# Kernel tuning notes

Measured on AMD Instinct MI355X. Metric: run time of the kernel, lower is better.

The kernel has to match this reference:

```python
import jax, jax.numpy as jnp
import numpy as np

B, S, H, NH = 4, 2048, 768, 12
HD = H // NH

def _ln(x, g, b, eps=1e-5):
    m = jnp.mean(x, -1, keepdims=True)
    v = jnp.mean((x - m) ** 2, -1, keepdims=True)
    return (x - m) * jax.lax.rsqrt(v + eps) * g + b

def setup_inputs() -> dict:
    key = jax.random.key(0)
    ks = jax.random.split(key, 16)
    s = 0.02
    return {
        "x": jax.random.normal(ks[0], (B, S, H), jnp.float32),
        "prev_state": jax.random.normal(ks[1], (B, S, H), jnp.float32),
        "mask": jax.random.randint(ks[2], (B,), 0, 2).astype(bool),
        # depthwise conv1d (groups=H, k=3): torch weight [H, 1, 3] == OIH
        "conv_dw_w": jax.random.normal(ks[3], (H, 1, 3), jnp.float32) * s,
        "conv_dw_b": jnp.zeros((H,), jnp.float32),
        # pointwise conv1d (k=1) stored as [out, in]
        "conv_pw_w": jax.random.normal(ks[4], (H, H), jnp.float32) * s,
        "conv_pw_b": jnp.zeros((H,), jnp.float32),
        "cn_g": jnp.ones((H,), jnp.float32), "cn_b": jnp.zeros((H,), jnp.float32),
        "Wq": jax.random.normal(ks[5], (H, H), jnp.float32) * s, "bq": jnp.zeros((H,), jnp.float32),
        "Wk": jax.random.normal(ks[6], (H, H), jnp.float32) * s, "bk": jnp.zeros((H,), jnp.float32),
        "Wv": jax.random.normal(ks[7], (H, H), jnp.float32) * s, "bv": jnp.zeros((H,), jnp.float32),
        "Wo": jax.random.normal(ks[8], (H, H), jnp.float32) * s, "bo": jnp.zeros((H,), jnp.float32),
        "pn_g": jnp.ones((H,), jnp.float32), "pn_b": jnp.zeros((H,), jnp.float32),
        "Wpost": jax.random.normal(ks[9], (H, H), jnp.float32) * s, "bpost": jnp.zeros((H,), jnp.float32),
        "Wg": jax.random.normal(ks[10], (1, 2 * H), jnp.float32) * s, "bg": jnp.zeros((1,), jnp.float32),
    }

def reference(x, prev_state, mask, conv_dw_w, conv_dw_b, conv_pw_w, conv_pw_b,
              cn_g, cn_b, Wq, bq, Wk, bk, Wv, bv, Wo, bo,
              pn_g, pn_b, Wpost, bpost, Wg, bg):
    # ---- bridge: depthwise conv (k=3) -> pointwise conv (k=1) -> GELU -> LN ----
    mem_t = prev_state.transpose(0, 2, 1)  # [B, H, S]
    dw = jax.lax.conv_general_dilated(
        mem_t, conv_dw_w, window_strides=(1,), padding=[(1, 1)],
        feature_group_count=H, dimension_numbers=("NCH", "OIH", "NCH")) + conv_dw_b[None, :, None]
    pw = jnp.einsum("bhs,oh->bos", dw, conv_pw_w) + conv_pw_b[None, :, None]
    bridged = jax.nn.gelu(pw, approximate=False).transpose(0, 2, 1)  # [B, S, H]
    bridged = _ln(bridged, cn_g, cn_b)
    # ---- cross attention: q from x, k/v from bridged memory (nope, non-causal) ----
    q = (jnp.einsum("bsh,oh->bso", x, Wq) + bq).reshape(B, S, NH, HD)
    k = (jnp.einsum("bsh,oh->bso", bridged, Wk) + bk).reshape(B, S, NH, HD)
    v = (jnp.einsum("bsh,oh->bso", bridged, Wv) + bv).reshape(B, S, NH, HD)
    scores = jnp.einsum("bqnd,bknd->bnqk", q, k) / np.float32(np.sqrt(HD))
    attn = jax.nn.softmax(scores, axis=-1)
    ao = jnp.einsum("bnqk,bknd->bqnd", attn, v).reshape(B, S, H)
    ao = jnp.einsum("bsh,oh->bso", ao, Wo) + bo
    # ---- post-attn norm, linear, gate, scatter-add back under mask ----
    inj = _ln(ao, pn_g, pn_b)
    inj = jnp.einsum("bsh,oh->bso", inj, Wpost) + bpost
    gate = jax.nn.sigmoid(jnp.einsum("bsh,oh->bso", jnp.concatenate([x, bridged], -1), Wg) + bg)
    gated = gate * jnp.tanh(inj)
    mf = mask.astype(x.dtype)[:, None, None]  # batch-row select == masked scatter-add
    out = x + mf * gated
    # masked MSE aux loss (only over selected rows, as in the original)
    denom = jnp.maximum(mask.sum(), 1).astype(x.dtype) * np.float32(S * H)
    aux = jnp.sum(mf * (bridged - x) ** 2) / denom
    return out, aux
```

## Files before the change

### kernel.cpp

```cpp
#include <hip/hip_runtime.h>
#include <math.h>

#define B_ 4
#define S_ 2048
#define H_ 768
#define NH_ 12
#define HD_ 64
#define BSH (B_ * S_ * H_)
#define NROWS (B_ * S_)
#define WSZ (H_ * H_)

typedef __attribute__((ext_vector_type(8))) short bf16x8;
typedef __attribute__((ext_vector_type(4))) short s16x4;
typedef __attribute__((ext_vector_type(4))) float f32x4;
typedef __attribute__((ext_vector_type(2))) unsigned u32x2;

__device__ __forceinline__ short f2bf(float f) {
  union { float f; unsigned u; } x; x.f = f;
  unsigned r = x.u + 0x7FFF + ((x.u >> 16) & 1);
  return (short)(r >> 16);
}
__device__ __forceinline__ float bf2f(short s) {
  union { unsigned u; float f; } x;
  x.u = ((unsigned)(unsigned short)s) << 16;
  return x.f;
}
__device__ __forceinline__ unsigned bfpack(float lo, float hi) {
  union { float f; unsigned u; } a, b; a.f = lo; b.f = hi;
  return __builtin_amdgcn_perm(b.u, a.u, 0x07060302);
}

typedef __attribute__((address_space(1))) const unsigned int g_u32;
typedef __attribute__((address_space(3))) unsigned int l_u32;
__device__ __forceinline__ void gload16(const void* g, void* l) {
  __builtin_amdgcn_global_load_lds((g_u32*)g, (l_u32*)l, 16, 0, 0);
}

__global__ __launch_bounds__(256) void cvt_x_k(const float* __restrict__ src,
                                               short* __restrict__ dst) {
  int i = (blockIdx.x * 256 + threadIdx.x) * 4;
  float4 v = *(const float4*)(src + i);
  s16x4 o = {f2bf(v.x), f2bf(v.y), f2bf(v.z), f2bf(v.w)};
  *(s16x4*)(dst + i) = o;
}

__global__ __launch_bounds__(256) void cvt6_k(const float* w0, const float* w1,
                                              const float* w2, const float* w3,
                                              const float* w4, const float* w5,
                                              short* __restrict__ dst) {
  int i = (blockIdx.x * 256 + threadIdx.x) * 4;
  int m = i / WSZ;
  int off = i - m * WSZ;
  const float* s = m == 0 ? w0 : m == 1 ? w1 : m == 2 ? w2 : m == 3 ? w3 : m == 4 ? w4 : w5;
  float4 v = *(const float4*)(s + off);
  s16x4 o = {f2bf(v.x), f2bf(v.y), f2bf(v.z), f2bf(v.w)};
  *(s16x4*)(dst + i) = o;
}

__global__ __launch_bounds__(192) void dwconv_k(const float* __restrict__ prev,
                                                const float* __restrict__ w3,
                                                const float* __restrict__ bias,
                                                short* __restrict__ out) {
  int row = blockIdx.x;
  int s = row & (S_ - 1);
  int h = threadIdx.x * 4;
  size_t base = (size_t)row * H_ + h;
  float4 c = *(const float4*)(prev + base);
  float4 wa = *(const float4*)(w3 + h * 3);
  float4 wb = *(const float4*)(w3 + h * 3 + 4);
  float4 wc = *(const float4*)(w3 + h * 3 + 8);
  float4 bi = *(const float4*)(bias + h);
  float4 acc;
  acc.x = bi.x + c.x * wa.y;
  acc.y = bi.y + c.y * wb.x;
  acc.z = bi.z + c.z * wb.w;
  acc.w = bi.w + c.w * wc.z;
  if (s > 0) {
    float4 l = *(const float4*)(prev + base - H_);
    acc.x += l.x * wa.x; acc.y += l.y * wa.w; acc.z += l.z * wb.z; acc.w += l.w * wc.y;
  }
  if (s < S_ - 1) {
    float4 r = *(const float4*)(prev + base + H_);
    acc.x += r.x * wa.z; acc.y += r.y * wb.y; acc.z += r.z * wc.x; acc.w += r.w * wc.w;
  }
  s16x4 o = {f2bf(acc.x), f2bf(acc.y), f2bf(acc.z), f2bf(acc.w)};
  *(s16x4*)(out + base) = o;
}

struct GemmJob {
  const short* A; const short* W; const float* bias; short* C; int act; int tout;
};

__global__ __launch_bounds__(256) void gemm_bf2(GemmJob j0, GemmJob j1, GemmJob j2) {
  GemmJob j = blockIdx.z == 0 ? j0 : (blockIdx.z == 1 ? j1 : j2);
  __shared__ short As[128 * 64];
  __shared__ short Ws[128 * 64];
  int tid = threadIdx.x, lane = tid & 63, w = tid >> 6;
  int wr = w >> 1, wc = w & 1, lm = lane & 15, lq = lane >> 4;
  int m0 = blockIdx.y * 128, n0 = blockIdx.x * 128;
  int srow = lane >> 3;
  int skc = (lane & 7) * 8;
  const short* gA = j.A + (size_t)(m0 + w * 32 + srow) * H_ + skc;
  const short* gW = j.W + (size_t)(n0 + w * 32 + srow) * H_ + skc;
  short* lA = As + w * 2048;
  short* lW = Ws + w * 2048;

  f32x4 acc[4][4];
#pragma unroll
  for (int i = 0; i < 4; ++i)
#pragma unroll
    for (int jj = 0; jj < 4; ++jj) acc[i][jj] = (f32x4){0.f, 0.f, 0.f, 0.f};

  for (int kt = 0; kt < H_; kt += 64) {
    __syncthreads();
#pragma unroll
    for (int c = 0; c < 4; ++c) {
      gload16(gA + kt + (size_t)(c * 8) * H_, lA + c * 512);
      gload16(gW + kt + (size_t)(c * 8) * H_, lW + c * 512);
    }
    __syncthreads();
#pragma unroll
    for (int kk = 0; kk < 2; ++kk) {
      bf16x8 af[4], wf[4];
#pragma unroll
      for (int i = 0; i < 4; ++i)
        af[i] = *(const bf16x8*)&As[(wr * 64 + i * 16 + lm) * 64 + kk * 32 + lq * 8];
#pragma unroll
      for (int jj = 0; jj < 4; ++jj)
        wf[jj] = *(const bf16x8*)&Ws[(wc * 64 + jj * 16 + lm) * 64 + kk * 32 + lq * 8];
#pragma unroll
      for (int i = 0; i < 4; ++i)
#pragma unroll
        for (int jj = 0; jj < 4; ++jj)
          acc[i][jj] = __builtin_amdgcn_mfma_f32_16x16x32_bf16(af[i], wf[jj], acc[i][jj], 0, 0, 0);
    }
  }

  if (!j.tout) {
#pragma unroll
    for (int jj = 0; jj < 4; ++jj) {
      int col = n0 + wc * 64 + jj * 16 + lm;
      float bn = j.bias[col];
#pragma unroll
      for (int i = 0; i < 4; ++i) {
        int mrow = m0 + wr * 64 + i * 16 + lq * 4;
#pragma unroll
        for (int r = 0; r < 4; ++r) {
          float cv = acc[i][jj][r] + bn;
          if (j.act) cv = 0.5f * cv * (1.0f + erff(cv * 0.70710678118f));
          j.C[(size_t)(mrow + r) * H_ + col] = f2bf(cv);
        }
      }
    }
  } else {
    int b = m0 >> 11;
    int sb = (m0 & (S_ - 1)) + wr * 64;
#pragma unroll
    for (int jj = 0; jj < 4; ++jj) {
      int col = n0 + wc * 64 + jj * 16 + lm;
      float bn = j.bias[col];
      short* cp = j.C + ((size_t)(b * H_ + col)) * S_;
#pragma unroll
      for (int i = 0; i < 4; ++i) {
        int s = sb + i * 16 + lq * 4;
        s16x4 pk = {f2bf(acc[i][jj][0] + bn), f2bf(acc[i][jj][1] + bn),
                    f2bf(acc[i][jj][2] + bn), f2bf(acc[i][jj][3] + bn)};
        *(s16x4*)(cp + s) = pk;
      }
    }
  }
}

__global__ __launch_bounds__(256) void gemm_n64(const short* __restrict__ A,
                                                const short* __restrict__ W,
                                                const float* __restrict__ bias,
                                                short* __restrict__ C, int act) {
  __shared__ short As[128 * 64];
  __shared__ short Ws[64 * 64];
  int tid = threadIdx.x, lane = tid & 63, w = tid >> 6;
  int wm = w >> 1, wn = w & 1, lm = lane & 15, lq = lane >> 4;
  int m0 = blockIdx.y * 128, n0 = blockIdx.x * 64;
  const short* gA = A + (size_t)(m0 + w * 32 + (lane >> 3)) * H_ + (lane & 7) * 8;
  const short* gW = W + (size_t)(n0 + w * 16 + (lane >> 3)) * H_ + (lane & 7) * 8;
  short* lA = As + w * 2048;
  short* lW = Ws + w * 1024;

  f32x4 acc[4][2];
#pragma unroll
  for (int i = 0; i < 4; ++i)
#pragma unroll
    for (int jj = 0; jj < 2; ++jj) acc[i][jj] = (f32x4){0.f, 0.f, 0.f, 0.f};

  for (int kt = 0; kt < H_; kt += 64) {
    __syncthreads();
#pragma unroll
    for (int c = 0; c < 4; ++c)
      gload16(gA + kt + (size_t)(c * 8) * H_, lA + c * 512);
#pragma unroll
    for (int c = 0; c < 2; ++c)
      gload16(gW + kt + (size_t)(c * 8) * H_, lW + c * 512);
    __syncthreads();
#pragma unroll
    for (int kk = 0; kk < 2; ++kk) {
      bf16x8 af[4], wf[2];
#pragma unroll
      for (int i = 0; i < 4; ++i)
        af[i] = *(const bf16x8*)&As[(wm * 64 + i * 16 + lm) * 64 + kk * 32 + lq * 8];
#pragma unroll
      for (int jj = 0; jj < 2; ++jj)
        wf[jj] = *(const bf16x8*)&Ws[(wn * 32 + jj * 16 + lm) * 64 + kk * 32 + lq * 8];
#pragma unroll
      for (int i = 0; i < 4; ++i)
#pragma unroll
        for (int jj = 0; jj < 2; ++jj)
          acc[i][jj] = __builtin_amdgcn_mfma_f32_16x16x32_bf16(af[i], wf[jj], acc[i][jj], 0, 0, 0);
    }
  }

#pragma unroll
  for (int jj = 0; jj < 2; ++jj) {
    int col = n0 + wn * 32 + jj * 16 + lm;
    float bn = bias[col];
#pragma unroll
    for (int i = 0; i < 4; ++i) {
      int mrow = m0 + wm * 64 + i * 16 + lq * 4;
#pragma unroll
      for (int r = 0; r < 4; ++r) {
        float cv = acc[i][jj][r] + bn;
        if (act) cv = 0.5f * cv * (1.0f + erff(cv * 0.70710678118f));
        C[(size_t)(mrow + r) * H_ + col] = f2bf(cv);
      }
    }
  }
}

__global__ __launch_bounds__(256) void ln_bf(const short* __restrict__ X,
                                             short* __restrict__ Y,
                                             const float* __restrict__ g,
                                             const float* __restrict__ bb) {
  int row = blockIdx.x;
  size_t base = (size_t)row * H_;
  int h0 = threadIdx.x, h1 = h0 + 256, h2 = h0 + 512;
  float x0 = bf2f(X[base + h0]), x1 = bf2f(X[base + h1]), x2 = bf2f(X[base + h2]);
  float s = x0 + x1 + x2;
  float s2 = x0 * x0 + x1 * x1 + x2 * x2;
  for (int off = 32; off > 0; off >>= 1) {
    s += __shfl_down(s, off);
    s2 += __shfl_down(s2, off);
  }
  __shared__ float sa[4], sq[4], st[2];
  int wid = threadIdx.x >> 6, lane = threadIdx.x & 63;
  if (lane == 0) { sa[wid] = s; sq[wid] = s2; }
  __syncthreads();
  if (threadIdx.x == 0) {
    float ts = sa[0] + sa[1] + sa[2] + sa[3];
    float ts2 = sq[0] + sq[1] + sq[2] + sq[3];
    float mean = ts * (1.0f / H_);
    float var = ts2 * (1.0f / H_) - mean * mean;
    st[0] = mean;
    st[1] = rsqrtf(var + 1e-5f);
  }
  __syncthreads();
  float mean = st[0], rstd = st[1];
  Y[base + h0] = f2bf((x0 - mean) * rstd * g[h0] + bb[h0]);
  Y[base + h1] = f2bf((x1 - mean) * rstd * g[h1] + bb[h1]);
  Y[base + h2] = f2bf((x2 - mean) * rstd * g[h2] + bb[h2]);
}

__global__ __launch_bounds__(256) void attn4_k(const short* __restrict__ qb,
                                               const short* __restrict__ kb,
                                               const short* __restrict__ vtb,
                                               short* __restrict__ aob) {
  __shared__ short Ks[64 * 72];
  __shared__ short Vt[64 * 72];
  __shared__ short Ps[128 * 72];
  int tid = threadIdx.x, lane = tid & 63, w = tid >> 6;
  int lm = lane & 15, lq = lane >> 4;
  int b = blockIdx.z, n = blockIdx.y, q0 = blockIdx.x * 128;
  int hoff = n * HD_;

  bf16x8 qf[2][2];
#pragma unroll
  for (int qg = 0; qg < 2; ++qg) {
    const short* qrow = qb + ((size_t)(b * S_ + q0 + w * 32 + qg * 16 + lm)) * H_ + hoff;
    qf[qg][0] = *(const bf16x8*)(qrow + lq * 8);
    qf[qg][1] = *(const bf16x8*)(qrow + 32 + lq * 8);
  }

  float l_[2] = {0.f, 0.f};
  f32x4 o[4][2];
#pragma unroll
  for (int i = 0; i < 4; ++i)
#pragma unroll
    for (int qg = 0; qg < 2; ++qg) o[i][qg] = (f32x4){0.f, 0.f, 0.f, 0.f};

  int r0 = tid >> 2, c0 = (tid & 3) * 16;
  const short* kg = kb + ((size_t)(b * S_)) * H_ + hoff;
  const short* vg = vtb + ((size_t)(b * H_ + hoff)) * S_;
  const float C1 = 0.1803368802f;

  bf16x8 kv0 = *(const bf16x8*)(kg + (size_t)r0 * H_ + c0);
  bf16x8 kv1 = *(const bf16x8*)(kg + (size_t)r0 * H_ + c0 + 8);
  bf16x8 vv0 = *(const bf16x8*)(vg + (size_t)r0 * S_ + c0);
  bf16x8 vv1 = *(const bf16x8*)(vg + (size_t)r0 * S_ + c0 + 8);

  for (int kt = 0; kt < S_; kt += 64) {
    __syncthreads();
    *(bf16x8*)&Ks[r0 * 72 + c0] = kv0;
    *(bf16x8*)&Ks[r0 * 72 + c0 + 8] = kv1;
    *(bf16x8*)&Vt[r0 * 72 + c0] = vv0;
    *(bf16x8*)&Vt[r0 * 72 + c0 + 8] = vv1;
    __syncthreads();
    if (kt + 64 < S_) {
      kv0 = *(const bf16x8*)(kg + (size_t)(kt + 64 + r0) * H_ + c0);
      kv1 = *(const bf16x8*)(kg + (size_t)(kt + 64 + r0) * H_ + c0 + 8);
      vv0 = *(const bf16x8*)(vg + (size_t)r0 * S_ + kt + 64 + c0);
      vv1 = *(const bf16x8*)(vg + (size_t)r0 * S_ + kt + 64 + c0 + 8);
    }

    f32x4 st[4][2];
#pragma unroll
    for (int ni = 0; ni < 4; ++ni) {
      bf16x8 ka0 = *(const bf16x8*)&Ks[(ni * 16 + lm) * 72 + lq * 8];
      bf16x8 ka1 = *(const bf16x8*)&Ks[(ni * 16 + lm) * 72 + 32 + lq * 8];
#pragma unroll
      for (int qg = 0; qg < 2; ++qg) {
        f32x4 z = (f32x4){0.f, 0.f, 0.f, 0.f};
        z = __builtin_amdgcn_mfma_f32_16x16x32_bf16(ka0, qf[qg][0], z, 0, 0, 0);
        st[ni][qg] = __builtin_amdgcn_mfma_f32_16x16x32_bf16(ka1, qf[qg][1], z, 0, 0, 0);
      }
    }

#pragma unroll
    for (int qg = 0; qg < 2; ++qg) {
      float rs = 0.f;
#pragma unroll
      for (int ni = 0; ni < 4; ++ni) {
        float p0 = exp2f(st[ni][qg][0] * C1);
        float p1 = exp2f(st[ni][qg][1] * C1);
        float p2 = exp2f(st[ni][qg][2] * C1);
        float p3 = exp2f(st[ni][qg][3] * C1);
        rs += (p0 + p1) + (p2 + p3);
        u32x2 pk = {bfpack(p0, p1), bfpack(p2, p3)};
        *(u32x2*)&Ps[(w * 32 + qg * 16 + lm) * 72 + ni * 16 + lq * 4] = pk;
      }
      rs += __shfl_xor(rs, 16);
      rs += __shfl_xor(rs, 32);
      l_[qg] += rs;
    }

    bf16x8 pf[2][2];
#pragma unroll
    for (int qg = 0; qg < 2; ++qg) {
      pf[qg][0] = *(const bf16x8*)&Ps[(w * 32 + qg * 16 + lm) * 72 + lq * 8];
      pf[qg][1] = *(const bf16x8*)&Ps[(w * 32 + qg * 16 + lm) * 72 + 32 + lq * 8];
    }
#pragma unroll
    for (int nd = 0; nd < 4; ++nd) {
      bf16x8 va0 = *(const bf16x8*)&Vt[(nd * 16 + lm) * 72 + lq * 8];
      bf16x8 va1 = *(const bf16x8*)&Vt[(nd * 16 + lm) * 72 + 32 + lq * 8];
#pragma unroll
      for (int qg = 0; qg < 2; ++qg) {
        o[nd][qg] = __builtin_amdgcn_mfma_f32_16x16x32_bf16(va0, pf[qg][0], o[nd][qg], 0, 0, 0);
        o[nd][qg] = __builtin_amdgcn_mfma_f32_16x16x32_bf16(va1, pf[qg][1], o[nd][qg], 0, 0, 0);
      }
    }
  }

#pragma unroll
  for (int qg = 0; qg < 2; ++qg) {
    float inv = 1.0f / l_[qg];
    short* orow = aob + ((size_t)(b * S_ + q0 + w * 32 + qg * 16 + lm)) * H_ + hoff;
#pragma unroll
    for (int nd = 0; nd < 4; ++nd) {
      s16x4 pk = {f2bf(o[nd][qg][0] * inv), f2bf(o[nd][qg][1] * inv),
                  f2bf(o[nd][qg][2] * inv), f2bf(o[nd][qg][3] * inv)};
      *(s16x4*)(orow + nd * 16 + lq * 4) = pk;
    }
  }
}

__global__ __launch_bounds__(192) void gate_out_k(const float* __restrict__ x,
                                                  const short* __restrict__ br,
                                                  const short* __restrict__ inj,
                                                  const int* __restrict__ mask,
                                                  const float* __restrict__ Wg,
                                                  const float* __restrict__ bg,
                                                  float* __restrict__ out,
                                                  float* __restrict__ paux) {
  int row = blockIdx.x;
  int b = row >> 11;
  size_t base = (size_t)row * H_;
  int h = threadIdx.x * 4;
  float4 xv = *(const float4*)(x + base + h);
  s16x4 brv = *(const s16x4*)(br + base + h);
  s16x4 inv = *(const s16x4*)(inj + base + h);
  float4 wg0 = *(const float4*)(Wg + h);
  float4 wg1 = *(const float4*)(Wg + H_ + h);
  float b0 = bf2f(brv.x), b1 = bf2f(brv.y), b2 = bf2f(brv.z), b3 = bf2f(brv.w);
  float dot = xv.x * wg0.x + xv.y * wg0.y + xv.z * wg0.z + xv.w * wg0.w
            + b0 * wg1.x + b1 * wg1.y + b2 * wg1.z + b3 * wg1.w;
  float d0 = b0 - xv.x, d1 = b1 - xv.y, d2 = b2 - xv.z, d3 = b3 - xv.w;
  float aux = d0 * d0 + d1 * d1 + d2 * d2 + d3 * d3;
  for (int off = 32; off > 0; off >>= 1) {
    dot += __shfl_down(dot, off);
    aux += __shfl_down(aux, off);
  }
  __shared__ float sd[3], sx[3], gsh[2];
  int wid = threadIdx.x >> 6, lane = threadIdx.x & 63;
  if (lane == 0) { sd[wid] = dot; sx[wid] = aux; }
  __syncthreads();
  if (threadIdx.x == 0) {
    float td = sd[0] + sd[1] + sd[2];
    float ta = sx[0] + sx[1] + sx[2];
    gsh[0] = 1.0f / (1.0f + expf(-(td + bg[0])));
    gsh[1] = ta;
  }
  __syncthreads();
  float mf = (mask[b] != 0) ? 1.0f : 0.0f;
  float gm = gsh[0] * mf;
  float v0 = bf2f(inv.x), v1 = bf2f(inv.y), v2 = bf2f(inv.z), v3 = bf2f(inv.w);
  float e0 = __expf(2.f * v0), e1 = __expf(2.f * v1), e2 = __expf(2.f * v2), e3 = __expf(2.f * v3);
  float4 ov;
  ov.x = xv.x + gm * ((e0 - 1.f) / (e0 + 1.f));
  ov.y = xv.y + gm * ((e1 - 1.f) / (e1 + 1.f));
  ov.z = xv.z + gm * ((e2 - 1.f) / (e2 + 1.f));
  ov.w = xv.w + gm * ((e3 - 1.f) / (e3 + 1.f));
  *(float4*)(out + base + h) = ov;
  if (threadIdx.x == 0) paux[row] = mf * gsh[1];
}

__global__ __launch_bounds__(256) void aux_reduce_k(const float* __restrict__ paux,
                                                    const int* __restrict__ mask,
                                                    float* __restrict__ outp) {
  float s = 0.f;
  for (int i = threadIdx.x; i < NROWS; i += 256) s += paux[i];
  for (int off = 32; off > 0; off >>= 1) s += __shfl_down(s, off);
  __shared__ float sw[4];
  int wid = threadIdx.x >> 6, lane = threadIdx.x & 63;
  if (lane == 0) sw[wid] = s;
  __syncthreads();
  if (threadIdx.x == 0) {
    float t = sw[0] + sw[1] + sw[2] + sw[3];
    int nm = (mask[0] != 0) + (mask[1] != 0) + (mask[2] != 0) + (mask[3] != 0);
    if (nm < 1) nm = 1;
    outp[0] = t / ((float)nm * (float)(S_ * H_));
  }
}

extern "C" void kernel_launch(void* const* d_in, const int* in_sizes, int n_in,
                              void* d_out, int out_size, void* d_ws, size_t ws_size,
                              hipStream_t stream) {
  const float* x     = (const float*)d_in[0];
  const float* prev  = (const float*)d_in[1];
  const int*   mask  = (const int*)d_in[2];
  const float* dw_w  = (const float*)d_in[3];
  const float* dw_b  = (const float*)d_in[4];
  const float* pw_w  = (const float*)d_in[5];
  const float* pw_b  = (const float*)d_in[6];
  const float* cn_g  = (const float*)d_in[7];
  const float* cn_b  = (const float*)d_in[8];
  const float* Wq    = (const float*)d_in[9];
  const float* bq    = (const float*)d_in[10];
  const float* Wk    = (const float*)d_in[11];
  const float* bk    = (const float*)d_in[12];
  const float* Wv    = (const float*)d_in[13];
  const float* bv    = (const float*)d_in[14];
  const float* Wo    = (const float*)d_in[15];
  const float* bo    = (const float*)d_in[16];
  const float* pn_g  = (const float*)d_in[17];
  const float* pn_b  = (const float*)d_in[18];
  const float* Wpost = (const float*)d_in[19];
  const float* bpost = (const float*)d_in[20];
  const float* Wg    = (const float*)d_in[21];
  const float* bg    = (const float*)d_in[22];
  float* out = (float*)d_out;

  short* B0 = (short*)d_ws;
  short* B1 = B0 + BSH;
  short* B2 = B1 + BSH;
  short* B3 = B2 + BSH;
  short* B4 = B3 + BSH;
  short* B5 = B4 + BSH;
  short* WW = B5 + BSH;
  float* paux = (float*)(WW + 6 * WSZ);

  dim3 g3(H_ / 128, NROWS / 128, 3);
  dim3 gn(H_ / 64, NROWS / 128, 1);

  GemmJob jq = {B0, WW + WSZ,     bq, B1, 0, 0};
  GemmJob jk = {B3, WW + 2 * WSZ, bk, B4, 0, 0};
  GemmJob jv = {B3, WW + 3 * WSZ, bv, B5, 0, 1};

  cvt6_k<<<6 * WSZ / 1024, 256, 0, stream>>>(pw_w, Wq, Wk, Wv, Wo, Wpost, WW);
  cvt_x_k<<<BSH / 1024, 256, 0, stream>>>(x, B0);
  dwconv_k<<<NROWS, 192, 0, stream>>>(prev, dw_w, dw_b, B1);
  gemm_n64<<<gn, 256, 0, stream>>>(B1, WW, pw_b, B2, 1);
  ln_bf<<<NROWS, 256, 0, stream>>>(B2, B3, cn_g, cn_b);
  gemm_bf2<<<g3, 256, 0, stream>>>(jq, jk, jv);
  attn4_k<<<dim3(S_ / 128, NH_, B_), 256, 0, stream>>>(B1, B4, B5, B2);
  gemm_n64<<<gn, 256, 0, stream>>>(B2, WW + 4 * WSZ, bo, B4, 0);
  ln_bf<<<NROWS, 256, 0, stream>>>(B4, B4, pn_g, pn_b);
  gemm_n64<<<gn, 256, 0, stream>>>(B4, WW + 5 * WSZ, bpost, B5, 0);
  gate_out_k<<<NROWS, 192, 0, stream>>>(x, B3, B5, mask, Wg, bg, out, paux);
  aux_reduce_k<<<1, 256, 0, stream>>>(paux, mask, out + BSH);
}
```

Baseline: 413.5 us.

## Replace GEMMs with register-prefetched 32x32 MFMA kernel, drop P round-trip in attention

Replaces both GEMM kernels with a single 128-thread kernel that uses 32x32x16 MFMA tiles, K-step 32, and register-staged prefetch of the next K slice instead of direct global-to-LDS loads. The Q projection now reads fp32 x directly and converts in-register, which removes the separate x conversion kernel. Attention switches to 16x16x16 MFMA so the softmax probabilities can stay in registers as operands, eliminating the Ps LDS buffer and its store/reload. LayerNorm is vectorized to 4 elements per thread with 192 threads. The smaller GEMM tiles and K-step mean more syncs and more redundant weight loads, and the attention change issues twice as many smaller MFMAs.

```diff
diff --git a/kernel.cpp b/kernel.cpp
--- a/kernel.cpp
+++ b/kernel.cpp
@@ -13,6 +13,7 @@
 typedef __attribute__((ext_vector_type(8))) short bf16x8;
 typedef __attribute__((ext_vector_type(4))) short s16x4;
 typedef __attribute__((ext_vector_type(4))) float f32x4;
+typedef __attribute__((ext_vector_type(16))) float f32x16;
 typedef __attribute__((ext_vector_type(2))) unsigned u32x2;
 
 __device__ __forceinline__ short f2bf(float f) {
@@ -29,19 +30,11 @@
   union { float f; unsigned u; } a, b; a.f = lo; b.f = hi;
   return __builtin_amdgcn_perm(b.u, a.u, 0x07060302);
 }
-
-typedef __attribute__((address_space(1))) const unsigned int g_u32;
-typedef __attribute__((address_space(3))) unsigned int l_u32;
-__device__ __forceinline__ void gload16(const void* g, void* l) {
-  __builtin_amdgcn_global_load_lds((g_u32*)g, (l_u32*)l, 16, 0, 0);
-}
-
-__global__ __launch_bounds__(256) void cvt_x_k(const float* __restrict__ src,
-                                               short* __restrict__ dst) {
-  int i = (blockIdx.x * 256 + threadIdx.x) * 4;
-  float4 v = *(const float4*)(src + i);
-  s16x4 o = {f2bf(v.x), f2bf(v.y), f2bf(v.z), f2bf(v.w)};
-  *(s16x4*)(dst + i) = o;
+__device__ __forceinline__ bf16x8 pack8(float4 a, float4 b) {
+  union { unsigned u[4]; bf16x8 v; } r;
+  r.u[0] = bfpack(a.x, a.y); r.u[1] = bfpack(a.z, a.w);
+  r.u[2] = bfpack(b.x, b.y); r.u[3] = bfpack(b.z, b.w);
+  return r.v;
 }
 
 __global__ __launch_bounds__(256) void cvt6_k(const float* w0, const float* w1,
@@ -87,174 +80,140 @@
   *(s16x4*)(out + base) = o;
 }
 
-struct GemmJob {
-  const short* A; const short* W; const float* bias; short* C; int act; int tout;
+struct GJob {
+  const void* A; const short* W; const float* bias; short* C;
+  int act; int tout; int af32;
 };
 
-__global__ __launch_bounds__(256) void gemm_bf2(GemmJob j0, GemmJob j1, GemmJob j2) {
-  GemmJob j = blockIdx.z == 0 ? j0 : (blockIdx.z == 1 ? j1 : j2);
-  __shared__ short As[128 * 64];
-  __shared__ short Ws[128 * 64];
+__global__ __launch_bounds__(128) void gemm32_k(GJob j0, GJob j1, GJob j2) {
+  GJob j = blockIdx.z == 0 ? j0 : (blockIdx.z == 1 ? j1 : j2);
+  __shared__ short As[128 * 32];
+  __shared__ short Ws[64 * 32];
   int tid = threadIdx.x, lane = tid & 63, w = tid >> 6;
-  int wr = w >> 1, wc = w & 1, lm = lane & 15, lq = lane >> 4;
-  int m0 = blockIdx.y * 128, n0 = blockIdx.x * 128;
-  int srow = lane >> 3;
-  int skc = (lane & 7) * 8;
-  const short* gA = j.A + (size_t)(m0 + w * 32 + srow) * H_ + skc;
-  const short* gW = j.W + (size_t)(n0 + w * 32 + srow) * H_ + skc;
-  short* lA = As + w * 2048;
-  short* lW = Ws + w * 2048;
-
-  f32x4 acc[4][4];
-#pragma unroll
-  for (int i = 0; i < 4; ++i)
-#pragma unroll
-    for (int jj = 0; jj < 4; ++jj) acc[i][jj] = (f32x4){0.f, 0.f, 0.f, 0.f};
-
-  for (int kt = 0; kt < H_; kt += 64) {
+  int l31 = lane & 31, half = lane >> 5;
+  int m0 = blockIdx.y * 128, n0 = blockIdx.x * 64;
+  int srow = tid >> 2;
+  int sc = (tid & 3) * 8;
+  const short* gA = (const short*)j.A + (size_t)(m0 + srow) * H_ + sc;
+  const float* gAf = (const float*)j.A + (size_t)(m0 + srow) * H_ + sc;
+  const short* gW = j.W + (size_t)(n0 + srow) * H_ + sc;
+
+  bf16x8 ra[4], rw[2];
+#pragma unroll
+  for (int p = 0; p < 4; ++p) {
+    if (j.af32) {
+      float4 f0 = *(const float4*)(gAf + (size_t)(p * 32) * H_);
+      float4 f1 = *(const float4*)(gAf + (size_t)(p * 32) * H_ + 4);
+      ra[p] = pack8(f0, f1);
+    } else {
+      ra[p] = *(const bf16x8*)(gA + (size_t)(p * 32) * H_);
+    }
+  }
+#pragma unroll
+  for (int p = 0; p < 2; ++p)
+    rw[p] = *(const bf16x8*)(gW + (size_t)(p * 32) * H_);
+
+  f32x16 acc[2][2];
+#pragma unroll
+  for (int i = 0; i < 2; ++i)
+#pragma unroll
+    for (int k = 0; k < 2; ++k) acc[i][k] = (f32x16)(0.f);
+
+  for (int kt = 0; kt < H_; kt += 32) {
     __syncthreads();
 #pragma unroll
-    for (int c = 0; c < 4; ++c) {
-      gload16(gA + kt + (size_t)(c * 8) * H_, lA + c * 512);
-      gload16(gW + kt + (size_t)(c * 8) * H_, lW + c * 512);
-    }
+    for (int p = 0; p < 4; ++p)
+      *(bf16x8*)&As[(p * 32 + srow) * 32 + sc] = ra[p];
+#pragma unroll
+    for (int p = 0; p < 2; ++p)
+      *(bf16x8*)&Ws[(p * 32 + srow) * 32 + sc] = rw[p];
     __syncthreads();
-#pragma unroll
-    for (int kk = 0; kk < 2; ++kk) {
-      bf16x8 af[4], wf[4];
-#pragma unroll
-      for (int i = 0; i < 4; ++i)
-        af[i] = *(const bf16x8*)&As[(wr * 64 + i * 16 + lm) * 64 + kk * 32 + lq * 8];
-#pragma unroll
-      for (int jj = 0; jj < 4; ++jj)
-        wf[jj] = *(const bf16x8*)&Ws[(wc * 64 + jj * 16 + lm) * 64 + kk * 32 + lq * 8];
-#pragma unroll
-      for (int i = 0; i < 4; ++i)
-#pragma unroll
-        for (int jj = 0; jj < 4; ++jj)
-          acc[i][jj] = __builtin_amdgcn_mfma_f32_16x16x32_bf16(af[i], wf[jj], acc[i][jj], 0, 0, 0);
-    }
-  }
-
-  if (!j.tout) {
-#pragma unroll
-    for (int jj = 0; jj < 4; ++jj) {
-      int col = n0 + wc * 64 + jj * 16 + lm;
-      float bn = j.bias[col];
-#pragma unroll
-      for (int i = 0; i < 4; ++i) {
-        int mrow = m0 + wr * 64 + i * 16 + lq * 4;
-#pragma unroll
-        for (int r = 0; r < 4; ++r) {
-          float cv = acc[i][jj][r] + bn;
-          if (j.act) cv = 0.5f * cv * (1.0f + erff(cv * 0.70710678118f));
-          j.C[(size_t)(mrow + r) * H_ + col] = f2bf(cv);
+    if (kt + 32 < H_) {
+      int k2 = kt + 32;
+#pragma unroll
+      for (int p = 0; p < 4; ++p) {
+        if (j.af32) {
+          float4 f0 = *(const float4*)(gAf + (size_t)(p * 32) * H_ + k2);
+          float4 f1 = *(const float4*)(gAf + (size_t)(p * 32) * H_ + k2 + 4);
+          ra[p] = pack8(f0, f1);
+        } else {
+          ra[p] = *(const bf16x8*)(gA + (size_t)(p * 32) * H_ + k2);
         }
       }
-    }
-  } else {
-    int b = m0 >> 11;
-    int sb = (m0 & (S_ - 1)) + wr * 64;
-#pragma unroll
-    for (int jj = 0; jj < 4; ++jj) {
-      int col = n0 + wc * 64 + jj * 16 + lm;
+#pragma unroll
+      for (int p = 0; p < 2; ++p)
+        rw[p] = *(const bf16x8*)(gW + (size_t)(p * 32) * H_ + k2);
+    }
+#pragma unroll
+    for (int kc = 0; kc < 2; ++kc) {
+      bf16x8 af[2], wf[2];
+#pragma unroll
+      for (int mi = 0; mi < 2; ++mi)
+        af[mi] = *(const bf16x8*)&As[(w * 64 + mi * 32 + l31) * 32 + kc * 16 + half * 8];
+#pragma unroll
+      for (int ni = 0; ni < 2; ++ni)
+        wf[ni] = *(const bf16x8*)&Ws[(ni * 32 + l31) * 32 + kc * 16 + half * 8];
+#pragma unroll
+      for (int mi = 0; mi < 2; ++mi)
+#pragma unroll
+        for (int ni = 0; ni < 2; ++ni)
+          acc[mi][ni] = __builtin_amdgcn_mfma_f32_32x32x16_bf16(af[mi], wf[ni], acc[mi][ni], 0, 0, 0);
+    }
+  }
+
+#pragma unroll
+  for (int mi = 0; mi < 2; ++mi) {
+#pragma unroll
+    for (int ni = 0; ni < 2; ++ni) {
+      int col = n0 + ni * 32 + l31;
       float bn = j.bias[col];
-      short* cp = j.C + ((size_t)(b * H_ + col)) * S_;
-#pragma unroll
-      for (int i = 0; i < 4; ++i) {
-        int s = sb + i * 16 + lq * 4;
-        s16x4 pk = {f2bf(acc[i][jj][0] + bn), f2bf(acc[i][jj][1] + bn),
-                    f2bf(acc[i][jj][2] + bn), f2bf(acc[i][jj][3] + bn)};
-        *(s16x4*)(cp + s) = pk;
+      if (!j.tout) {
+        int rbase = m0 + w * 64 + mi * 32 + half * 4;
+#pragma unroll
+        for (int q = 0; q < 4; ++q)
+#pragma unroll
+          for (int r = 0; r < 4; ++r) {
+            float cv = acc[mi][ni][q * 4 + r] + bn;
+            if (j.act) cv = 0.5f * cv * (1.0f + erff(cv * 0.70710678118f));
+            j.C[(size_t)(rbase + q * 8 + r) * H_ + col] = f2bf(cv);
+          }
+      } else {
+        int bb = m0 >> 11;
+        int sb = (m0 & (S_ - 1)) + w * 64 + mi * 32 + half * 4;
+        short* cp = j.C + ((size_t)(bb * H_ + col)) * S_;
+#pragma unroll
+        for (int q = 0; q < 4; ++q) {
+          s16x4 pk = {f2bf(acc[mi][ni][q * 4 + 0] + bn), f2bf(acc[mi][ni][q * 4 + 1] + bn),
+                      f2bf(acc[mi][ni][q * 4 + 2] + bn), f2bf(acc[mi][ni][q * 4 + 3] + bn)};
+          *(s16x4*)(cp + sb + q * 8) = pk;
+        }
       }
     }
   }
 }
 
-__global__ __launch_bounds__(256) void gemm_n64(const short* __restrict__ A,
-                                                const short* __restrict__ W,
-                                                const float* __restrict__ bias,
-                                                short* __restrict__ C, int act) {
-  __shared__ short As[128 * 64];
-  __shared__ short Ws[64 * 64];
-  int tid = threadIdx.x, lane = tid & 63, w = tid >> 6;
-  int wm = w >> 1, wn = w & 1, lm = lane & 15, lq = lane >> 4;
-  int m0 = blockIdx.y * 128, n0 = blockIdx.x * 64;
-  const short* gA = A + (size_t)(m0 + w * 32 + (lane >> 3)) * H_ + (lane & 7) * 8;
-  const short* gW = W + (size_t)(n0 + w * 16 + (lane >> 3)) * H_ + (lane & 7) * 8;
-  short* lA = As + w * 2048;
-  short* lW = Ws + w * 1024;
-
-  f32x4 acc[4][2];
-#pragma unroll
-  for (int i = 0; i < 4; ++i)
-#pragma unroll
-    for (int jj = 0; jj < 2; ++jj) acc[i][jj] = (f32x4){0.f, 0.f, 0.f, 0.f};
-
-  for (int kt = 0; kt < H_; kt += 64) {
-    __syncthreads();
-#pragma unroll
-    for (int c = 0; c < 4; ++c)
-      gload16(gA + kt + (size_t)(c * 8) * H_, lA + c * 512);
-#pragma unroll
-    for (int c = 0; c < 2; ++c)
-      gload16(gW + kt + (size_t)(c * 8) * H_, lW + c * 512);
-    __syncthreads();
-#pragma unroll
-    for (int kk = 0; kk < 2; ++kk) {
-      bf16x8 af[4], wf[2];
-#pragma unroll
-      for (int i = 0; i < 4; ++i)
-        af[i] = *(const bf16x8*)&As[(wm * 64 + i * 16 + lm) * 64 + kk * 32 + lq * 8];
-#pragma unroll
-      for (int jj = 0; jj < 2; ++jj)
-        wf[jj] = *(const bf16x8*)&Ws[(wn * 32 + jj * 16 + lm) * 64 + kk * 32 + lq * 8];
-#pragma unroll
-      for (int i = 0; i < 4; ++i)
-#pragma unroll
-        for (int jj = 0; jj < 2; ++jj)
-          acc[i][jj] = __builtin_amdgcn_mfma_f32_16x16x32_bf16(af[i], wf[jj], acc[i][jj], 0, 0, 0);
-    }
-  }
-
-#pragma unroll
-  for (int jj = 0; jj < 2; ++jj) {
-    int col = n0 + wn * 32 + jj * 16 + lm;
-    float bn = bias[col];
-#pragma unroll
-    for (int i = 0; i < 4; ++i) {
-      int mrow = m0 + wm * 64 + i * 16 + lq * 4;
-#pragma unroll
-      for (int r = 0; r < 4; ++r) {
-        float cv = acc[i][jj][r] + bn;
-        if (act) cv = 0.5f * cv * (1.0f + erff(cv * 0.70710678118f));
-        C[(size_t)(mrow + r) * H_ + col] = f2bf(cv);
-      }
-    }
-  }
-}
-
-__global__ __launch_bounds__(256) void ln_bf(const short* __restrict__ X,
+__global__ __launch_bounds__(192) void ln_bf(const short* __restrict__ X,
                                              short* __restrict__ Y,
                                              const float* __restrict__ g,
                                              const float* __restrict__ bb) {
   int row = blockIdx.x;
   size_t base = (size_t)row * H_;
-  int h0 = threadIdx.x, h1 = h0 + 256, h2 = h0 + 512;
-  float x0 = bf2f(X[base + h0]), x1 = bf2f(X[base + h1]), x2 = bf2f(X[base + h2]);
-  float s = x0 + x1 + x2;
-  float s2 = x0 * x0 + x1 * x1 + x2 * x2;
+  int h = threadIdx.x * 4;
+  s16x4 xv = *(const s16x4*)(X + base + h);
+  float x0 = bf2f(xv.x), x1 = bf2f(xv.y), x2 = bf2f(xv.z), x3 = bf2f(xv.w);
+  float s = (x0 + x1) + (x2 + x3);
+  float s2 = (x0 * x0 + x1 * x1) + (x2 * x2 + x3 * x3);
   for (int off = 32; off > 0; off >>= 1) {
     s += __shfl_down(s, off);
     s2 += __shfl_down(s2, off);
   }
-  __shared__ float sa[4], sq[4], st[2];
+  __shared__ float sa[3], sq[3], st[2];
   int wid = threadIdx.x >> 6, lane = threadIdx.x & 63;
   if (lane == 0) { sa[wid] = s; sq[wid] = s2; }
   __syncthreads();
   if (threadIdx.x == 0) {
-    float ts = sa[0] + sa[1] + sa[2] + sa[3];
-    float ts2 = sq[0] + sq[1] + sq[2] + sq[3];
+    float ts = sa[0] + sa[1] + sa[2];
+    float ts2 = sq[0] + sq[1] + sq[2];
     float mean = ts * (1.0f / H_);
     float var = ts2 * (1.0f / H_) - mean * mean;
     st[0] = mean;
@@ -262,29 +221,33 @@
   }
   __syncthreads();
   float mean = st[0], rstd = st[1];
-  Y[base + h0] = f2bf((x0 - mean) * rstd * g[h0] + bb[h0]);
-  Y[base + h1] = f2bf((x1 - mean) * rstd * g[h1] + bb[h1]);
-  Y[base + h2] = f2bf((x2 - mean) * rstd * g[h2] + bb[h2]);
-}
-
-__global__ __launch_bounds__(256) void attn4_k(const short* __restrict__ qb,
+  float4 gg = *(const float4*)(g + h);
+  float4 bv = *(const float4*)(bb + h);
+  s16x4 o = {f2bf((x0 - mean) * rstd * gg.x + bv.x),
+             f2bf((x1 - mean) * rstd * gg.y + bv.y),
+             f2bf((x2 - mean) * rstd * gg.z + bv.z),
+             f2bf((x3 - mean) * rstd * gg.w + bv.w)};
+  *(s16x4*)(Y + base + h) = o;
+}
+
+__global__ __launch_bounds__(256) void attn5_k(const short* __restrict__ qb,
                                                const short* __restrict__ kb,
                                                const short* __restrict__ vtb,
                                                short* __restrict__ aob) {
   __shared__ short Ks[64 * 72];
   __shared__ short Vt[64 * 72];
-  __shared__ short Ps[128 * 72];
   int tid = threadIdx.x, lane = tid & 63, w = tid >> 6;
   int lm = lane & 15, lq = lane >> 4;
   int b = blockIdx.z, n = blockIdx.y, q0 = blockIdx.x * 128;
   int hoff = n * HD_;
 
-  bf16x8 qf[2][2];
+  s16x4 qf[2][4];
 #pragma unroll
   for (int qg = 0; qg < 2; ++qg) {
     const short* qrow = qb + ((size_t)(b * S_ + q0 + w * 32 + qg * 16 + lm)) * H_ + hoff;
-    qf[qg][0] = *(const bf16x8*)(qrow + lq * 8);
-    qf[qg][1] = *(const bf16x8*)(qrow + 32 + lq * 8);
+#pragma unroll
+    for (int dc = 0; dc < 4; ++dc)
+      qf[qg][dc] = *(const s16x4*)(qrow + dc * 16 + lq * 4);
   }
 
   float l_[2] = {0.f, 0.f};
@@ -321,16 +284,18 @@
     f32x4 st[4][2];
 #pragma unroll
     for (int ni = 0; ni < 4; ++ni) {
-      bf16x8 ka0 = *(const bf16x8*)&Ks[(ni * 16 + lm) * 72 + lq * 8];
-      bf16x8 ka1 = *(const bf16x8*)&Ks[(ni * 16 + lm) * 72 + 32 + lq * 8];
-#pragma unroll
-      for (int qg = 0; qg < 2; ++qg) {
-        f32x4 z = (f32x4){0.f, 0.f, 0.f, 0.f};
-        z = __builtin_amdgcn_mfma_f32_16x16x32_bf16(ka0, qf[qg][0], z, 0, 0, 0);
-        st[ni][qg] = __builtin_amdgcn_mfma_f32_16x16x32_bf16(ka1, qf[qg][1], z, 0, 0, 0);
+#pragma unroll
+      for (int qg = 0; qg < 2; ++qg) st[ni][qg] = (f32x4){0.f, 0.f, 0.f, 0.f};
+#pragma unroll
+      for (int dc = 0; dc < 4; ++dc) {
+        s16x4 ka = *(const s16x4*)&Ks[(ni * 16 + lm) * 72 + dc * 16 + lq * 4];
+#pragma unroll
+        for (int qg = 0; qg < 2; ++qg)
+          st[ni][qg] = __builtin_amdgcn_mfma_f32_16x16x16bf16_1k(ka, qf[qg][dc], st[ni][qg], 0, 0, 0);
       }
     }
 
+    s16x4 ppk[4][2];
 #pragma unroll
     for (int qg = 0; qg < 2; ++qg) {
       float rs = 0.f;
@@ -341,28 +306,23 @@
         float p2 = exp2f(st[ni][qg][2] * C1);
         float p3 = exp2f(st[ni][qg][3] * C1);
         rs += (p0 + p1) + (p2 + p3);
-        u32x2 pk = {bfpack(p0, p1), bfpack(p2, p3)};
-        *(u32x2*)&Ps[(w * 32 + qg * 16 + lm) * 72 + ni * 16 + lq * 4] = pk;
+        union { u32x2 u; s16x4 s; } pk;
+        pk.u = (u32x2){bfpack(p0, p1), bfpack(p2, p3)};
+        ppk[ni][qg] = pk.s;
       }
       rs += __shfl_xor(rs, 16);
       rs += __shfl_xor(rs, 32);
       l_[qg] += rs;
     }
 
-    bf16x8 pf[2][2];
-#pragma unroll
-    for (int qg = 0; qg < 2; ++qg) {
-      pf[qg][0] = *(const bf16x8*)&Ps[(w * 32 + qg * 16 + lm) * 72 + lq * 8];
-      pf[qg][1] = *(const bf16x8*)&Ps[(w * 32 + qg * 16 + lm) * 72 + 32 + lq * 8];
-    }
 #pragma unroll
     for (int nd = 0; nd < 4; ++nd) {
-      bf16x8 va0 = *(const bf16x8*)&Vt[(nd * 16 + lm) * 72 + lq * 8];
-      bf16x8 va1 = *(const bf16x8*)&Vt[(nd * 16 + lm) * 72 + 32 + lq * 8];
-#pragma unroll
-      for (int qg = 0; qg < 2; ++qg) {
-        o[nd][qg] = __builtin_amdgcn_mfma_f32_16x16x32_bf16(va0, pf[qg][0], o[nd][qg], 0, 0, 0);
-        o[nd][qg] = __builtin_amdgcn_mfma_f32_16x16x32_bf16(va1, pf[qg][1], o[nd][qg], 0, 0, 0);
+#pragma unroll
+      for (int ni = 0; ni < 4; ++ni) {
+        s16x4 va = *(const s16x4*)&Vt[(nd * 16 + lm) * 72 + ni * 16 + lq * 4];
+#pragma unroll
+        for (int qg = 0; qg < 2; ++qg)
+          o[nd][qg] = __builtin_amdgcn_mfma_f32_16x16x16bf16_1k(va, ppk[ni][qg], o[nd][qg], 0, 0, 0);
       }
     }
   }
@@ -485,23 +445,25 @@
   short* WW = B5 + BSH;
   float* paux = (float*)(WW + 6 * WSZ);
 
-  dim3 g3(H_ / 128, NROWS / 128, 3);
-  dim3 gn(H_ / 64, NROWS / 128, 1);
-
-  GemmJob jq = {B0, WW + WSZ,     bq, B1, 0, 0};
-  GemmJob jk = {B3, WW + 2 * WSZ, bk, B4, 0, 0};
-  GemmJob jv = {B3, WW + 3 * WSZ, bv, B5, 0, 1};
+  dim3 g1(H_ / 64, NROWS / 128, 1);
+  dim3 g3(H_ / 64, NROWS / 128, 3);
+
+  GJob jpw   = {B1, WW,           pw_b,  B2, 1, 0, 0};
+  GJob jq    = {x,  WW + WSZ,     bq,    B1, 0, 0, 1};
+  GJob jk    = {B3, WW + 2 * WSZ, bk,    B4, 0, 0, 0};
+  GJob jv    = {B3, WW + 3 * WSZ, bv,    B5, 0, 1, 0};
+  GJob jo    = {B2, WW + 4 * WSZ, bo,    B4, 0, 0, 0};
+  GJob jpost = {B4, WW + 5 * WSZ, bpost, B5, 0, 0, 0};
 
   cvt6_k<<<6 * WSZ / 1024, 256, 0, stream>>>(pw_w, Wq, Wk, Wv, Wo, Wpost, WW);
-  cvt_x_k<<<BSH / 1024, 256, 0, stream>>>(x, B0);
   dwconv_k<<<NROWS, 192, 0, stream>>>(prev, dw_w, dw_b, B1);
-  gemm_n64<<<gn, 256, 0, stream>>>(B1, WW, pw_b, B2, 1);
-  ln_bf<<<NROWS, 256, 0, stream>>>(B2, B3, cn_g, cn_b);
-  gemm_bf2<<<g3, 256, 0, stream>>>(jq, jk, jv);
-  attn4_k<<<dim3(S_ / 128, NH_, B_), 256, 0, stream>>>(B1, B4, B5, B2);
-  gemm_n64<<<gn, 256, 0, stream>>>(B2, WW + 4 * WSZ, bo, B4, 0);
-  ln_bf<<<NROWS, 256, 0, stream>>>(B4, B4, pn_g, pn_b);
-  gemm_n64<<<gn, 256, 0, stream>>>(B4, WW + 5 * WSZ, bpost, B5, 0);
+  gemm32_k<<<g1, 128, 0, stream>>>(jpw, jpw, jpw);
+  ln_bf<<<NROWS, 192, 0, stream>>>(B2, B3, cn_g, cn_b);
+  gemm32_k<<<g3, 128, 0, stream>>>(jq, jk, jv);
+  attn5_k<<<dim3(S_ / 128, NH_, B_), 256, 0, stream>>>(B1, B4, B5, B2);
+  gemm32_k<<<g1, 128, 0, stream>>>(jo, jo, jo);
+  ln_bf<<<NROWS, 192, 0, stream>>>(B4, B4, pn_g, pn_b);
+  gemm32_k<<<g1, 128, 0, stream>>>(jpost, jpost, jpost);
   gate_out_k<<<NROWS, 192, 0, stream>>>(x, B3, B5, mask, Wg, bg, out, paux);
   aux_reduce_k<<<1, 256, 0, stream>>>(paux, mask, out + BSH);
 }
```

Result: slower. 478.7 us (+15.8%).
